# Performance work log

Hardware: AMD Instinct MI355X
Metric: run time of the kernel (lower is better)

## Reference

```python
import jax, jax.numpy as jnp
import numpy as np

N_NODES = 100000
N_EDGES = 1600000
NODE_DIM = 128
EDGE_DIM = 32
GLOBAL_DIM = 64
HIDDEN_DIM = 256
N_GRAPHS = 512
IN_DIM = NODE_DIM + EDGE_DIM + GLOBAL_DIM  # 224


def setup_inputs() -> dict:
    key = jax.random.key(0)
    ks = jax.random.split(key, 10)
    x = jax.random.normal(ks[0], (N_NODES, NODE_DIM), dtype=jnp.float32)
    edge_index = jax.random.randint(ks[1], (2, N_EDGES), 0, N_NODES, dtype=jnp.int64)
    edge_attr = jax.random.normal(ks[2], (N_EDGES, EDGE_DIM), dtype=jnp.float32)
    u = jax.random.normal(ks[3], (N_GRAPHS, GLOBAL_DIM), dtype=jnp.float32)
    batch = jnp.sort(jax.random.randint(ks[4], (N_NODES,), 0, N_GRAPHS, dtype=jnp.int64))
    s1 = 1.0 / np.sqrt(IN_DIM)
    s2 = 1.0 / np.sqrt(HIDDEN_DIM)
    W1 = jax.random.uniform(ks[5], (IN_DIM, HIDDEN_DIM), jnp.float32, -s1, s1)
    b1 = jnp.zeros((HIDDEN_DIM,), jnp.float32)
    W2 = jax.random.uniform(ks[6], (HIDDEN_DIM, HIDDEN_DIM), jnp.float32, -s2, s2)
    b2 = jnp.zeros((HIDDEN_DIM,), jnp.float32)
    W3 = jax.random.uniform(ks[7], (HIDDEN_DIM, GLOBAL_DIM), jnp.float32, -s2, s2)
    b3 = jnp.zeros((GLOBAL_DIM,), jnp.float32)
    return {"x": x, "edge_index": edge_index, "edge_attr": edge_attr, "u": u,
            "batch": batch, "W1": W1, "b1": b1, "W2": W2, "b2": b2, "W3": W3, "b3": b3}


def _scatter_mean(vals, seg_ids, num_segments):
    # vals: [M, D], seg_ids: [M] -> [num_segments, D]
    sums = jax.ops.segment_sum(vals, seg_ids, num_segments=num_segments)
    cnt = jax.ops.segment_sum(jnp.ones((vals.shape[0],), vals.dtype), seg_ids,
                              num_segments=num_segments)
    return sums / jnp.maximum(cnt, 1.0)[:, None]


def reference(x, edge_index, edge_attr, u, batch, W1, b1, W2, b2, W3, b3):
    B = u.shape[0]
    node_mean = _scatter_mean(x, batch, B)                      # [B, node_dim]
    edge_seg = batch[edge_index[0]]                             # [E]
    edge_mean = _scatter_mean(edge_attr, edge_seg, B)           # [B, edge_dim]
    out = jnp.concatenate([node_mean, edge_mean, u], axis=1)    # [B, in_dim]
    h = jax.nn.relu(out @ W1 + b1)
    h = jax.nn.relu(h @ W2 + b2)
    return h @ W3 + b3                                          # [B, global_dim]
```

## Files before the change

### kernel.cpp

```cpp
#include <hip/hip_runtime.h>
#include <hip/hip_bf16.h>

#define N_NODES    100000
#define N_EDGES    1600000
#define NODE_DIM   128
#define EDGE_DIM   32
#define GLOBAL_DIM 64
#define HIDDEN_DIM 256
#define N_GRAPHS   512
#define IN_DIM     224
#define ROW33      33

#define EDGE_BLKS  256
#define EDGE_CH    (N_EDGES / EDGE_BLKS)
#define SLOTSZ     (N_GRAPHS * ROW33)
#define GPB        2

#define FXS   1048576.0f
#define FXINV (1.0f / 1048576.0f)

#define WS_NSUM   0
#define WS_NCNT   (WS_NSUM + N_GRAPHS * NODE_DIM)
#define WS_ESLOT  (WS_NCNT + N_GRAPHS)

__global__ __launch_bounds__(1024) void bulk(const float* __restrict__ eattr,
                                             const int* __restrict__ eidx,
                                             const float* __restrict__ x,
                                             const int* __restrict__ batch,
                                             int* __restrict__ eslot,
                                             float* __restrict__ nsum,
                                             float* __restrict__ ncnt) {
    __shared__ int ssum[SLOTSZ];
    const int t = threadIdx.x;

    if (blockIdx.x < EDGE_BLKS) {
        for (int i = t; i < SLOTSZ; i += 1024) ssum[i] = 0;
        __syncthreads();

        const float4* eattr4 = reinterpret_cast<const float4*>(eattr);
        const int p = t & 7;
        const int e1 = blockIdx.x * EDGE_CH + EDGE_CH;
        int e = blockIdx.x * EDGE_CH + (t >> 3);

        int    s_nxt = (e < e1) ? batch[eidx[e]] : 0;
        float4 v_nxt = (e < e1) ? eattr4[(size_t)e * 8 + p] : float4{0.f, 0.f, 0.f, 0.f};

#pragma unroll 2
        for (; e < e1; e += 128) {
            const int s = s_nxt;
            const float4 v = v_nxt;
            const int en = e + 128;
            if (en < e1) {
                s_nxt = batch[eidx[en]];
                v_nxt = eattr4[(size_t)en * 8 + p];
            }
            const int b = s * ROW33 + p * 4;
            atomicAdd(&ssum[b + 0], __float2int_rn(v.x * FXS));
            atomicAdd(&ssum[b + 1], __float2int_rn(v.y * FXS));
            atomicAdd(&ssum[b + 2], __float2int_rn(v.z * FXS));
            atomicAdd(&ssum[b + 3], __float2int_rn(v.w * FXS));
            if (p == 0) atomicAdd(&ssum[s * ROW33 + 32], 1);
        }
        __syncthreads();

        int* gs = eslot + (size_t)blockIdx.x * SLOTSZ;
        for (int i = t; i < SLOTSZ; i += 1024) gs[i] = ssum[i];
    } else {
        const int g = blockIdx.x - EDGE_BLKS;
        __shared__ int sb[2];
        if (t < 2) {
            const int target = g + t;
            int lo = 0, hi = N_NODES;
            while (lo < hi) {
                const int mid = (lo + hi) >> 1;
                if (batch[mid] < target) lo = mid + 1; else hi = mid;
            }
            sb[t] = lo;
        }
        __syncthreads();
        const int s0 = sb[0], e0 = sb[1];

        const int dp = t & 63;
        const int off = t >> 6;
        float ax0 = 0.f, ay0 = 0.f, ax1 = 0.f, ay1 = 0.f;
        float ax2 = 0.f, ay2 = 0.f, ax3 = 0.f, ay3 = 0.f;
        int r = s0 + off;
        for (; r + 48 < e0; r += 64) {
            const float2 v0 = *reinterpret_cast<const float2*>(x + (size_t)(r     ) * NODE_DIM + dp * 2);
            const float2 v1 = *reinterpret_cast<const float2*>(x + (size_t)(r + 16) * NODE_DIM + dp * 2);
            const float2 v2 = *reinterpret_cast<const float2*>(x + (size_t)(r + 32) * NODE_DIM + dp * 2);
            const float2 v3 = *reinterpret_cast<const float2*>(x + (size_t)(r + 48) * NODE_DIM + dp * 2);
            ax0 += v0.x; ay0 += v0.y; ax1 += v1.x; ay1 += v1.y;
            ax2 += v2.x; ay2 += v2.y; ax3 += v3.x; ay3 += v3.y;
        }
        for (; r < e0; r += 16) {
            const float2 v = *reinterpret_cast<const float2*>(x + (size_t)r * NODE_DIM + dp * 2);
            ax0 += v.x; ay0 += v.y;
        }

        float2* part2 = reinterpret_cast<float2*>(ssum);
        part2[t] = float2{(ax0 + ax1) + (ax2 + ax3), (ay0 + ay1) + (ay2 + ay3)};
        __syncthreads();
        if (t < 64) {
            float sx = 0.f, sy = 0.f;
#pragma unroll 16
            for (int k = 0; k < 16; ++k) {
                const float2 v = part2[t + 64 * k];
                sx += v.x; sy += v.y;
            }
            reinterpret_cast<float2*>(nsum)[(size_t)g * 64 + t] = float2{sx, sy};
        }
        if (t == 0) ncnt[g] = fmaxf((float)(e0 - s0), 1.f);
    }
}

__global__ __launch_bounds__(256) void finalize_mlp(const float* __restrict__ nsum,
                                                    const float* __restrict__ ncnt,
                                                    const int* __restrict__ eslot,
                                                    const float* __restrict__ u,
                                                    const float* __restrict__ W1, const float* __restrict__ b1,
                                                    const float* __restrict__ W2, const float* __restrict__ b2,
                                                    const float* __restrict__ W3, const float* __restrict__ b3,
                                                    float* __restrict__ out) {
    const int g0 = blockIdx.x * GPB;
    const int t = threadIdx.x;
    __shared__ float fs[GPB * IN_DIM];
    __shared__ long long redll[256];
    __shared__ long long redcnt[8];
    __shared__ float h[GPB][HIDDEN_DIM];
    __shared__ float h2[GPB][HIDDEN_DIM];
    __shared__ float red[GPB][256];
    __shared__ float s_ecnt[GPB];

    {
        const int col = t & 63, part = t >> 6;
        const int g = col >> 5, d = col & 31;
        long long s = 0;
#pragma unroll 8
        for (int sl = part * 64; sl < part * 64 + 64; ++sl)
            s += eslot[(size_t)sl * SLOTSZ + (size_t)(g0 + g) * ROW33 + d];
        redll[t] = s;
    }
    if (t < 8) {
        const int g = t & 1, part = t >> 1;
        long long c = 0;
#pragma unroll 8
        for (int sl = part * 64; sl < part * 64 + 64; ++sl)
            c += eslot[(size_t)sl * SLOTSZ + (size_t)(g0 + g) * ROW33 + 32];
        redcnt[t] = c;
    }
    __syncthreads();
    if (t < GPB)
        s_ecnt[t] = fmaxf((float)(redcnt[t] + redcnt[t + 2] + redcnt[t + 4] + redcnt[t + 6]), 1.f);

    {
        const int g = t >> 7, d = t & 127;
        fs[g * IN_DIM + d] = nsum[(size_t)(g0 + g) * NODE_DIM + d] / ncnt[g0 + g];
    }
    __syncthreads();
    if (t < 64) {
        const long long tot = redll[t] + redll[t + 64] + redll[t + 128] + redll[t + 192];
        const int g = t >> 5, d = t & 31;
        fs[g * IN_DIM + NODE_DIM + d] = ((float)tot * FXINV) / s_ecnt[g];
    } else if (t < 192) {
        const int i = t - 64, g = i >> 6, c = i & 63;
        fs[g * IN_DIM + NODE_DIM + EDGE_DIM + c] = u[(size_t)(g0 + g) * GLOBAL_DIM + c];
    }
    __syncthreads();

    float acc0, acc1;
    const float bb1 = b1[t];
    acc0 = acc1 = bb1;
    for (int k = 0; k < IN_DIM; ++k) {
        const float w = W1[k * HIDDEN_DIM + t];
        acc0 = fmaf(fs[k], w, acc0);
        acc1 = fmaf(fs[IN_DIM + k], w, acc1);
    }
    h[0][t] = fmaxf(acc0, 0.f); h[1][t] = fmaxf(acc1, 0.f);
    __syncthreads();

    const float bb2 = b2[t];
    acc0 = acc1 = bb2;
    for (int k = 0; k < HIDDEN_DIM; ++k) {
        const float w = W2[k * HIDDEN_DIM + t];
        acc0 = fmaf(h[0][k], w, acc0);
        acc1 = fmaf(h[1][k], w, acc1);
    }
    h2[0][t] = fmaxf(acc0, 0.f); h2[1][t] = fmaxf(acc1, 0.f);
    __syncthreads();

    const int c3 = t & 63, q = t >> 6;
    acc0 = acc1 = 0.f;
    for (int k = q * 64; k < q * 64 + 64; ++k) {
        const float w = W3[k * GLOBAL_DIM + c3];
        acc0 = fmaf(h2[0][k], w, acc0);
        acc1 = fmaf(h2[1][k], w, acc1);
    }
    red[0][t] = acc0; red[1][t] = acc1;
    __syncthreads();
    if (t < GPB * GLOBAL_DIM) {
        const int g = t >> 6, c = t & 63;
        out[(size_t)(g0 + g) * GLOBAL_DIM + c] = red[g][c] + red[g][c + 64] +
                                                 red[g][c + 128] + red[g][c + 192] + b3[c];
    }
}

extern "C" void kernel_launch(void* const* d_in, const int* in_sizes, int n_in,
                              void* d_out, int out_size, void* d_ws, size_t ws_size,
                              hipStream_t stream) {
    const float* x         = (const float*)d_in[0];
    const int*   edge_idx  = (const int*)d_in[1];
    const float* edge_attr = (const float*)d_in[2];
    const float* u         = (const float*)d_in[3];
    const int*   batch     = (const int*)d_in[4];
    const float* W1 = (const float*)d_in[5];
    const float* b1 = (const float*)d_in[6];
    const float* W2 = (const float*)d_in[7];
    const float* b2 = (const float*)d_in[8];
    const float* W3 = (const float*)d_in[9];
    const float* b3 = (const float*)d_in[10];
    float* out = (float*)d_out;

    int* ws32 = (int*)d_ws;
    float* nsum  = (float*)(ws32 + WS_NSUM);
    float* ncnt  = (float*)(ws32 + WS_NCNT);
    int*   eslot = ws32 + WS_ESLOT;

    bulk<<<EDGE_BLKS + N_GRAPHS, 1024, 0, stream>>>(edge_attr, edge_idx, x, batch,
                                                    eslot, nsum, ncnt);
    finalize_mlp<<<N_GRAPHS / GPB, 256, 0, stream>>>(nsum, ncnt, eslot, u,
                                                     W1, b1, W2, b2, W3, b3, out);
}
```

Before: 90.92 us.

## Double edge blocks, widen per-thread edge and node loads to two float4s

Edge accumulation now uses 512 blocks, with each thread handling 8 features (two float4 loads) of an edge, so 256 edges are processed per iteration. The node-mean path switches from float2 to float4 loads with 32 threads per row and a 32-way shared reduction. The finalize kernel sums 512 slot partials instead of 256. The goal is more parallelism and wider memory transactions in the bulk kernel. In exchange the partial-slot buffer doubles, so more memory traffic and reduction work land in finalize_mlp, and there is more per-thread atomic contention.

```diff
diff --git a/kernel.cpp b/kernel.cpp
--- a/kernel.cpp
+++ b/kernel.cpp
@@ -11,7 +11,7 @@
 #define IN_DIM     224
 #define ROW33      33
 
-#define EDGE_BLKS  256
+#define EDGE_BLKS  512
 #define EDGE_CH    (N_EDGES / EDGE_BLKS)
 #define SLOTSZ     (N_GRAPHS * ROW33)
 #define GPB        2
@@ -38,27 +38,36 @@
         __syncthreads();
 
         const float4* eattr4 = reinterpret_cast<const float4*>(eattr);
-        const int p = t & 7;
+        const int p = t & 3;
         const int e1 = blockIdx.x * EDGE_CH + EDGE_CH;
-        int e = blockIdx.x * EDGE_CH + (t >> 3);
-
-        int    s_nxt = (e < e1) ? batch[eidx[e]] : 0;
-        float4 v_nxt = (e < e1) ? eattr4[(size_t)e * 8 + p] : float4{0.f, 0.f, 0.f, 0.f};
-
-#pragma unroll 2
-        for (; e < e1; e += 128) {
+        int e = blockIdx.x * EDGE_CH + (t >> 2);
+
+        int s_nxt = 0;
+        float4 va_nxt = float4{0.f, 0.f, 0.f, 0.f}, vb_nxt = va_nxt;
+        if (e < e1) {
+            s_nxt  = batch[eidx[e]];
+            va_nxt = eattr4[(size_t)e * 8 + p * 2];
+            vb_nxt = eattr4[(size_t)e * 8 + p * 2 + 1];
+        }
+
+        for (; e < e1; e += 256) {
             const int s = s_nxt;
-            const float4 v = v_nxt;
-            const int en = e + 128;
+            const float4 va = va_nxt, vb = vb_nxt;
+            const int en = e + 256;
             if (en < e1) {
-                s_nxt = batch[eidx[en]];
-                v_nxt = eattr4[(size_t)en * 8 + p];
+                s_nxt  = batch[eidx[en]];
+                va_nxt = eattr4[(size_t)en * 8 + p * 2];
+                vb_nxt = eattr4[(size_t)en * 8 + p * 2 + 1];
             }
-            const int b = s * ROW33 + p * 4;
-            atomicAdd(&ssum[b + 0], __float2int_rn(v.x * FXS));
-            atomicAdd(&ssum[b + 1], __float2int_rn(v.y * FXS));
-            atomicAdd(&ssum[b + 2], __float2int_rn(v.z * FXS));
-            atomicAdd(&ssum[b + 3], __float2int_rn(v.w * FXS));
+            const int b = s * ROW33 + p * 8;
+            atomicAdd(&ssum[b + 0], __float2int_rn(va.x * FXS));
+            atomicAdd(&ssum[b + 1], __float2int_rn(va.y * FXS));
+            atomicAdd(&ssum[b + 2], __float2int_rn(va.z * FXS));
+            atomicAdd(&ssum[b + 3], __float2int_rn(va.w * FXS));
+            atomicAdd(&ssum[b + 4], __float2int_rn(vb.x * FXS));
+            atomicAdd(&ssum[b + 5], __float2int_rn(vb.y * FXS));
+            atomicAdd(&ssum[b + 6], __float2int_rn(vb.z * FXS));
+            atomicAdd(&ssum[b + 7], __float2int_rn(vb.w * FXS));
             if (p == 0) atomicAdd(&ssum[s * ROW33 + 32], 1);
         }
         __syncthreads();
@@ -80,35 +89,33 @@
         __syncthreads();
         const int s0 = sb[0], e0 = sb[1];
 
-        const int dp = t & 63;
-        const int off = t >> 6;
-        float ax0 = 0.f, ay0 = 0.f, ax1 = 0.f, ay1 = 0.f;
-        float ax2 = 0.f, ay2 = 0.f, ax3 = 0.f, ay3 = 0.f;
+        const int dq = t & 31;
+        const int off = t >> 5;
+        float4 a0 = float4{0.f, 0.f, 0.f, 0.f}, a1 = a0;
         int r = s0 + off;
-        for (; r + 48 < e0; r += 64) {
-            const float2 v0 = *reinterpret_cast<const float2*>(x + (size_t)(r     ) * NODE_DIM + dp * 2);
-            const float2 v1 = *reinterpret_cast<const float2*>(x + (size_t)(r + 16) * NODE_DIM + dp * 2);
-            const float2 v2 = *reinterpret_cast<const float2*>(x + (size_t)(r + 32) * NODE_DIM + dp * 2);
-            const float2 v3 = *reinterpret_cast<const float2*>(x + (size_t)(r + 48) * NODE_DIM + dp * 2);
-            ax0 += v0.x; ay0 += v0.y; ax1 += v1.x; ay1 += v1.y;
-            ax2 += v2.x; ay2 += v2.y; ax3 += v3.x; ay3 += v3.y;
-        }
-        for (; r < e0; r += 16) {
-            const float2 v = *reinterpret_cast<const float2*>(x + (size_t)r * NODE_DIM + dp * 2);
-            ax0 += v.x; ay0 += v.y;
-        }
-
-        float2* part2 = reinterpret_cast<float2*>(ssum);
-        part2[t] = float2{(ax0 + ax1) + (ax2 + ax3), (ay0 + ay1) + (ay2 + ay3)};
-        __syncthreads();
-        if (t < 64) {
-            float sx = 0.f, sy = 0.f;
-#pragma unroll 16
-            for (int k = 0; k < 16; ++k) {
-                const float2 v = part2[t + 64 * k];
-                sx += v.x; sy += v.y;
+        for (; r + 32 < e0; r += 64) {
+            const float4 v0 = *reinterpret_cast<const float4*>(x + (size_t)(r     ) * NODE_DIM + dq * 4);
+            const float4 v1 = *reinterpret_cast<const float4*>(x + (size_t)(r + 32) * NODE_DIM + dq * 4);
+            a0.x += v0.x; a0.y += v0.y; a0.z += v0.z; a0.w += v0.w;
+            a1.x += v1.x; a1.y += v1.y; a1.z += v1.z; a1.w += v1.w;
+        }
+        for (; r < e0; r += 32) {
+            const float4 v = *reinterpret_cast<const float4*>(x + (size_t)r * NODE_DIM + dq * 4);
+            a0.x += v.x; a0.y += v.y; a0.z += v.z; a0.w += v.w;
+        }
+        a0.x += a1.x; a0.y += a1.y; a0.z += a1.z; a0.w += a1.w;
+
+        float4* part4 = reinterpret_cast<float4*>(ssum);
+        part4[t] = a0;
+        __syncthreads();
+        if (t < 32) {
+            float4 s = float4{0.f, 0.f, 0.f, 0.f};
+#pragma unroll 32
+            for (int k = 0; k < 32; ++k) {
+                const float4 v = part4[t + 32 * k];
+                s.x += v.x; s.y += v.y; s.z += v.z; s.w += v.w;
             }
-            reinterpret_cast<float2*>(nsum)[(size_t)g * 64 + t] = float2{sx, sy};
+            reinterpret_cast<float4*>(nsum)[(size_t)g * 32 + t] = s;
         }
         if (t == 0) ncnt[g] = fmaxf((float)(e0 - s0), 1.f);
     }
@@ -137,7 +144,7 @@
         const int g = col >> 5, d = col & 31;
         long long s = 0;
 #pragma unroll 8
-        for (int sl = part * 64; sl < part * 64 + 64; ++sl)
+        for (int sl = part * 128; sl < part * 128 + 128; ++sl)
             s += eslot[(size_t)sl * SLOTSZ + (size_t)(g0 + g) * ROW33 + d];
         redll[t] = s;
     }
@@ -145,7 +152,7 @@
         const int g = t & 1, part = t >> 1;
         long long c = 0;
 #pragma unroll 8
-        for (int sl = part * 64; sl < part * 64 + 64; ++sl)
+        for (int sl = part * 128; sl < part * 128 + 128; ++sl)
             c += eslot[(size_t)sl * SLOTSZ + (size_t)(g0 + g) * ROW33 + 32];
         redcnt[t] = c;
     }
```

Result: slower. 95.46 us (+5.0%).
